# Optimization experiments

Measured on AMD Instinct MI355X. Metric: run time of the kernel, lower is better.

The kernel has to match this reference:

```python
import jax, jax.numpy as jnp
import numpy as np

NUM_CLASSES = 20   # M = len(unique(true)); label 0 is background (skipped)
ALPHA = 0.7
BETA = 1.5


def setup_inputs() -> dict:
    key = jax.random.key(0)
    k1, k2, k3 = jax.random.split(key, 3)
    B, N, K = 1, 262144, 128
    points = jax.random.normal(k1, (B, N, 3), dtype=jnp.float32)
    true = jax.random.randint(k2, (B, N), 0, NUM_CLASSES)
    embedding = jax.random.normal(k3, (B, N, K), dtype=jnp.float32)
    return {"points": points, "true": true, "embedding": embedding}


def reference(points, true, embedding):
    # points: (B,N,3), true: (B,N) int labels in [0,M), embedding: (B,N,K). B == 1.
    B, N, K = embedding.shape
    M = NUM_CLASSES
    t = true[0]  # (N,)

    # g = sigmoid(||p||) per point
    g = jax.nn.sigmoid(jnp.sqrt(jnp.sum(points ** 2, axis=-1)))  # (B,N)

    # per-cluster counts and embedding means (segment reduce over N)
    counts = jax.ops.segment_sum(jnp.ones((N,), points.dtype), t, num_segments=M)  # (M,)
    safe_counts = jnp.maximum(counts, 1.0)
    means = jax.ops.segment_sum(embedding[0], t, num_segments=M) / safe_counts[:, None]  # (M,K)

    # intra-cluster: per point, distance to its cluster mean
    d = jnp.sqrt(jnp.sum((embedding - means[true]) ** 2, axis=-1))  # (B,N)
    per_point = g * jnp.square(jnp.maximum(d - ALPHA, 0.0))         # (B,N)
    intra_per_cluster = jax.ops.segment_sum(per_point[0], t, num_segments=M) / safe_counts  # (M,)
    intra = jnp.sum(intra_per_cluster[1:])  # sum over clusters 1..M-1 (skip background 0)

    # inter-cluster: pairwise mean distances among foreground clusters
    me = means[1:]                                    # (M-1, K)
    sq = jnp.sum((me[:, None, :] - me[None, :, :]) ** 2, axis=-1)  # (M-1, M-1)
    eye = jnp.eye(M - 1, dtype=sq.dtype)
    dist = jnp.sqrt(jnp.where(eye > 0, 1.0, sq))      # safe sqrt on diagonal
    inter = jnp.sum((1.0 - eye) * jnp.square(jnp.maximum(BETA - dist, 0.0)))

    return jnp.broadcast_to(intra / M + inter / (M * (M - 1)), (B,))
```

## Files before the change

kernel.cpp:

```cpp
#include <hip/hip_runtime.h>
#include <hip/hip_bf16.h>
#include <math.h>

#define NCLS 20
#define KDIM 128
#define ALPHA 0.7f
#define BETA 1.5f

#define WS_SUMS 0
#define WS_CNT (NCLS * KDIM)
#define WS_INTRA (NCLS * KDIM + NCLS)
#define WS_HIST (NCLS * KDIM + 2 * NCLS)
#define WS_CUR (NCLS * KDIM + 3 * NCLS)
#define WS_ZERO 4096
#define WS_PAIRS 4096
#define WS_NEEDED ((WS_PAIRS + 2 * 262144) * 4)

#define GRID 2048

__global__ void k_init(float* ws) {
    int i = blockIdx.x * blockDim.x + threadIdx.x;
    if (i < WS_ZERO) ws[i] = 0.0f;
}

__global__ void __launch_bounds__(256) k_hist(const int4* __restrict__ t4,
                                              float* __restrict__ ws, int N4) {
    __shared__ int h[NCLS];
    const int tid = threadIdx.x;
    if (tid < NCLS) h[tid] = 0;
    __syncthreads();
    const int gid = blockIdx.x * 256 + tid;
    if (gid < N4) {
        const int4 c = t4[gid];
        atomicAdd(&h[c.x], 1);
        atomicAdd(&h[c.y], 1);
        atomicAdd(&h[c.z], 1);
        atomicAdd(&h[c.w], 1);
    }
    __syncthreads();
    if (tid < NCLS) atomicAdd((int*)&ws[WS_HIST] + tid, h[tid]);
}

__global__ void k_scan(float* __restrict__ ws) {
    if (threadIdx.x == 0) {
        const int* h = (const int*)&ws[WS_HIST];
        int* cur = (int*)&ws[WS_CUR];
        int run = 0;
        for (int c = 0; c < NCLS; c++) {
            cur[c] = run;
            ws[WS_CNT + c] = (float)h[c];
            run += h[c];
        }
    }
}

__global__ void __launch_bounds__(256) k_scatter(const int4* __restrict__ t4,
                                                 float* __restrict__ ws, int N4) {
    __shared__ int h[NCLS], lbase[NCLS], lcur[NCLS];
    const int tid = threadIdx.x;
    if (tid < NCLS) { h[tid] = 0; lcur[tid] = 0; }
    __syncthreads();
    const int gid = blockIdx.x * 256 + tid;
    int4 c4 = make_int4(0, 0, 0, 0);
    if (gid < N4) {
        c4 = t4[gid];
        atomicAdd(&h[c4.x], 1);
        atomicAdd(&h[c4.y], 1);
        atomicAdd(&h[c4.z], 1);
        atomicAdd(&h[c4.w], 1);
    }
    __syncthreads();
    if (tid < NCLS) lbase[tid] = atomicAdd((int*)&ws[WS_CUR] + tid, h[tid]);
    __syncthreads();
    if (gid < N4) {
        int2* pairs = (int2*)&ws[WS_PAIRS];
        const int p0 = gid * 4;
        int cc[4] = {c4.x, c4.y, c4.z, c4.w};
        for (int j = 0; j < 4; j++) {
            const int c = cc[j];
            const int dst = lbase[c] + atomicAdd(&lcur[c], 1);
            pairs[dst] = make_int2(c, p0 + j);
        }
    }
}

#define SUMS_GRID 1024
__global__ void __launch_bounds__(256) k_sums(const float4* __restrict__ emb4,
                                              const float* __restrict__ ws_ro,
                                              float* __restrict__ ws, int N) {
    __shared__ float lsum[NCLS * KDIM];
    const int tid = threadIdx.x;
    for (int i = tid; i < NCLS * KDIM; i += 256) lsum[i] = 0.0f;
    __syncthreads();

    const int s = tid & 31;
    const int hw = blockIdx.x * 8 + (tid >> 5);
    const int2* pairs = (const int2*)&ws_ro[WS_PAIRS];
    const int base = hw * 32;

#define FLUSHA(C, A)                                                \
    {                                                               \
        float* a = &lsum[(C) * KDIM + 4 * s];                       \
        unsafeAtomicAdd(a + 0, (A).x);                              \
        unsafeAtomicAdd(a + 1, (A).y);                              \
        unsafeAtomicAdd(a + 2, (A).z);                              \
        unsafeAtomicAdd(a + 3, (A).w);                              \
    }

    if (base < N) {
        int2 pr = pairs[base];
        int ccur = __builtin_amdgcn_readfirstlane(pr.x);
        float4 acc = emb4[(size_t)pr.y * 32 + s];
        for (int j0 = 4; j0 <= 32; j0 += 4) {
            int2 q0, q1, q2, q3;
            float4 v0, v1, v2, v3;
            const bool more = j0 < 32;
            if (more) {
                q0 = pairs[base + j0 + 0];
                q1 = pairs[base + j0 + 1];
                q2 = pairs[base + j0 + 2];
                q3 = pairs[base + j0 + 3];
                v0 = emb4[(size_t)q0.y * 32 + s];
                v1 = emb4[(size_t)q1.y * 32 + s];
                v2 = emb4[(size_t)q2.y * 32 + s];
                v3 = emb4[(size_t)q3.y * 32 + s];
            }
            const int lo = j0 - 4 ? j0 - 4 : 1;
            for (int j = lo; j < j0; j++) {
                int2 q = pairs[base + j];
                float4 v = emb4[(size_t)q.y * 32 + s];
                const int c = __builtin_amdgcn_readfirstlane(q.x);
                if (c != ccur) {
                    FLUSHA(ccur, acc);
                    ccur = c;
                    acc = v;
                } else {
                    acc.x += v.x; acc.y += v.y; acc.z += v.z; acc.w += v.w;
                }
            }
            (void)more; (void)q0; (void)q1; (void)q2; (void)q3;
            (void)v0; (void)v1; (void)v2; (void)v3;
        }
        FLUSHA(ccur, acc);
    }
#undef FLUSHA
    __syncthreads();

    for (int i = tid; i < NCLS * KDIM; i += 256)
        if (lsum[i] != 0.0f) unsafeAtomicAdd(&ws[WS_SUMS + i], lsum[i]);
}

#define FB_BLK 128
#define FB_GRID 2048
__global__ void __launch_bounds__(FB_BLK) k_sums_fb(const float4* __restrict__ emb4,
                                                    const int* __restrict__ t,
                                                    float* __restrict__ ws, int N) {
    __shared__ float lsum[2][NCLS * KDIM];
    __shared__ float lcnt[NCLS];
    __shared__ int lds_t[FB_BLK];
    const int tid = threadIdx.x;
    const int w = tid >> 6, k = tid & 63;
    const int half = k >> 5;
    const int k31 = k & 31;
    for (int i = tid; i < 2 * NCLS * KDIM; i += FB_BLK) (&lsum[0][0])[i] = 0.0f;
    if (tid < NCLS) lcnt[tid] = 0.0f;
    __syncthreads();
    const int chunk = blockIdx.x * FB_BLK;
    const int npts = min(FB_BLK, N - chunk);
    if (tid < npts) {
        const int c = t[chunk + tid];
        lds_t[tid] = c;
        unsafeAtomicAdd(&lcnt[c], 1.0f);
    }
    __syncthreads();
    float* L = lsum[w];
    for (int q = 32 * w; q < 32 * w + 32; q++) {
        const int pl = 2 * q + half;
        if (pl < npts) {
            const int c = lds_t[pl];
            const float4 v = emb4[(size_t)(chunk + pl) * 32 + k31];
            const int cA = __shfl(c, 0, 64);
            const int cB = __shfl(c, 32, 64);
            if (cA == cB) {
                float4 vv;
                vv.x = v.x + __shfl_xor(v.x, 32, 64);
                vv.y = v.y + __shfl_xor(v.y, 32, 64);
                vv.z = v.z + __shfl_xor(v.z, 32, 64);
                vv.w = v.w + __shfl_xor(v.w, 32, 64);
                if (half == 0) {
                    float4* a = (float4*)&L[cA * KDIM + 4 * k31];
                    float4 o = *a;
                    o.x += vv.x; o.y += vv.y; o.z += vv.z; o.w += vv.w;
                    *a = o;
                }
            } else {
                float4* a = (float4*)&L[c * KDIM + 4 * k31];
                float4 o = *a;
                o.x += v.x; o.y += v.y; o.z += v.z; o.w += v.w;
                *a = o;
            }
        }
    }
    __syncthreads();
    for (int i = tid; i < NCLS * KDIM; i += FB_BLK)
        unsafeAtomicAdd(&ws[WS_SUMS + i], lsum[0][i] + lsum[1][i]);
    if (tid < NCLS) unsafeAtomicAdd(&ws[WS_CNT + tid], lcnt[tid]);
}

__global__ void __launch_bounds__(256) k_intra(const float4* __restrict__ emb4,
                                               const int* __restrict__ t,
                                               const float* __restrict__ pts,
                                               float* __restrict__ ws, int N) {
    __shared__ float lmean[NCLS * KDIM];
    __shared__ float lintra[NCLS];
    const int tid = threadIdx.x;
    for (int i = tid; i < NCLS * KDIM; i += 256) {
        float cnt = ws[WS_CNT + i / KDIM];
        lmean[i] = ws[WS_SUMS + i] / fmaxf(cnt, 1.0f);
    }
    if (tid < NCLS) lintra[tid] = 0.0f;
    __syncthreads();

    const int s = tid & 31;
    const int pp = tid >> 5;
    const int stride = GRID * 8;
    for (int p = blockIdx.x * 8 + pp; p < N; p += 2 * stride) {
        const int p1 = p + stride;
        {
            const int c = t[p];
            const float4 v = emb4[(size_t)p * 32 + s];
            const float4 m = *(const float4*)&lmean[c * KDIM + 4 * s];
            float dx = v.x - m.x, dy = v.y - m.y, dz = v.z - m.z, dw = v.w - m.w;
            float d2 = dx * dx + dy * dy + dz * dz + dw * dw;
            for (int off = 16; off >= 1; off >>= 1) d2 += __shfl_down(d2, off, 32);
            if (s == 0) {
                float d = sqrtf(d2);
                float px = pts[(size_t)p * 3 + 0];
                float py = pts[(size_t)p * 3 + 1];
                float pz = pts[(size_t)p * 3 + 2];
                float r = sqrtf(px * px + py * py + pz * pz);
                float g = 1.0f / (1.0f + expf(-r));
                float h = fmaxf(d - ALPHA, 0.0f);
                unsafeAtomicAdd(&lintra[c], g * h * h);
            }
        }
        if (p1 < N) {
            const int c = t[p1];
            const float4 v = emb4[(size_t)p1 * 32 + s];
            const float4 m = *(const float4*)&lmean[c * KDIM + 4 * s];
            float dx = v.x - m.x, dy = v.y - m.y, dz = v.z - m.z, dw = v.w - m.w;
            float d2 = dx * dx + dy * dy + dz * dz + dw * dw;
            for (int off = 16; off >= 1; off >>= 1) d2 += __shfl_down(d2, off, 32);
            if (s == 0) {
                float d = sqrtf(d2);
                float px = pts[(size_t)p1 * 3 + 0];
                float py = pts[(size_t)p1 * 3 + 1];
                float pz = pts[(size_t)p1 * 3 + 2];
                float r = sqrtf(px * px + py * py + pz * pz);
                float g = 1.0f / (1.0f + expf(-r));
                float h = fmaxf(d - ALPHA, 0.0f);
                unsafeAtomicAdd(&lintra[c], g * h * h);
            }
        }
    }
    __syncthreads();
    if (tid < NCLS) unsafeAtomicAdd(&ws[WS_INTRA + tid], lintra[tid]);
}

__global__ void __launch_bounds__(256) k_final(const float* __restrict__ ws,
                                               float* __restrict__ out) {
    __shared__ float lmean[NCLS * KDIM];
    __shared__ float red[256];
    const int tid = threadIdx.x;
    for (int i = tid; i < NCLS * KDIM; i += 256) {
        float cnt = ws[WS_CNT + i / KDIM];
        lmean[i] = ws[WS_SUMS + i] / fmaxf(cnt, 1.0f);
    }
    __syncthreads();

    float acc = 0.0f;
    for (int idx = tid; idx < 361; idx += 256) {
        int i = idx / 19 + 1;
        int j = idx % 19 + 1;
        if (i != j) {
            float sq = 0.0f;
            const float* mi = lmean + i * KDIM;
            const float* mj = lmean + j * KDIM;
            for (int k = 0; k < KDIM; k++) {
                float df = mi[k] - mj[k];
                sq += df * df;
            }
            float dist = sqrtf(sq);
            float h = fmaxf(BETA - dist, 0.0f);
            acc += h * h;
        }
    }
    red[tid] = acc;
    __syncthreads();
    for (int st = 128; st >= 1; st >>= 1) {
        if (tid < st) red[tid] += red[tid + st];
        __syncthreads();
    }
    if (tid == 0) {
        float intra = 0.0f;
        for (int c = 1; c < NCLS; c++) {
            intra += ws[WS_INTRA + c] / fmaxf(ws[WS_CNT + c], 1.0f);
        }
        out[0] = intra / (float)NCLS + red[0] / (float)(NCLS * (NCLS - 1));
    }
}

extern "C" void kernel_launch(void* const* d_in, const int* in_sizes, int n_in,
                              void* d_out, int out_size, void* d_ws, size_t ws_size,
                              hipStream_t stream) {
    const float* pts = (const float*)d_in[0];
    const int* t = (const int*)d_in[1];
    const int4* t4 = (const int4*)d_in[1];
    const float4* emb4 = (const float4*)d_in[2];
    float* out = (float*)d_out;
    float* ws = (float*)d_ws;
    const int N = in_sizes[1];
    const int N4 = N / 4;

    k_init<<<(WS_ZERO + 255) / 256, 256, 0, stream>>>(ws);

    if (ws_size >= (size_t)WS_NEEDED && (N % 4) == 0) {
        k_hist<<<(N4 + 255) / 256, 256, 0, stream>>>(t4, ws, N4);
        k_scan<<<1, 64, 0, stream>>>(ws);
        k_scatter<<<(N4 + 255) / 256, 256, 0, stream>>>(t4, ws, N4);
        k_sums<<<SUMS_GRID, 256, 0, stream>>>(emb4, ws, ws, N);
    } else {
        k_sums_fb<<<FB_GRID, FB_BLK, 0, stream>>>(emb4, t, ws, N);
    }
    k_intra<<<GRID, 256, 0, stream>>>(emb4, t, pts, ws, N);
    k_final<<<1, 256, 0, stream>>>(ws, out);
}
```

Baseline: 106.3 us.

## Rewrite sorted segment-sum to shuffle-broadcast pairs and flush directly to global

The sorted-pairs segment-sum kernel no longer uses a shared-memory accumulator. Each lane loads one (class, index) pair once and broadcasts it with shuffles, and gathers are issued eight at a time so more loads are in flight. Run boundaries are flushed with atomics straight to global sums. This drops the LDS zeroing, the final LDS-to-global pass and the redundant per-lane pair loads, at the cost of more global atomics at class boundaries. The scan is also parallelised across threads, the init kernel becomes a single small block, and restrict qualifiers on the aliased workspace are removed.

Result: slower. 185.8 us (+74.9%).

```diff
diff --git a/kernel.cpp b/kernel.cpp
--- a/kernel.cpp
+++ b/kernel.cpp
@@ -9,18 +9,18 @@
 
 #define WS_SUMS 0
 #define WS_CNT (NCLS * KDIM)
-#define WS_INTRA (NCLS * KDIM + NCLS)
-#define WS_HIST (NCLS * KDIM + 2 * NCLS)
-#define WS_CUR (NCLS * KDIM + 3 * NCLS)
-#define WS_ZERO 4096
+#define WS_INTRA (WS_CNT + NCLS)
+#define WS_HIST (WS_INTRA + NCLS)
+#define WS_CUR (WS_HIST + NCLS)
+#define WS_ZERO_N (WS_CUR + NCLS)
 #define WS_PAIRS 4096
 #define WS_NEEDED ((WS_PAIRS + 2 * 262144) * 4)
 
 #define GRID 2048
 
 __global__ void k_init(float* ws) {
-    int i = blockIdx.x * blockDim.x + threadIdx.x;
-    if (i < WS_ZERO) ws[i] = 0.0f;
+    const int tid = threadIdx.x;
+    for (int i = tid; i < WS_ZERO_N; i += 256) ws[i] = 0.0f;
 }
 
 __global__ void __launch_bounds__(256) k_hist(const int4* __restrict__ t4,
@@ -41,21 +41,19 @@
     if (tid < NCLS) atomicAdd((int*)&ws[WS_HIST] + tid, h[tid]);
 }
 
-__global__ void k_scan(float* __restrict__ ws) {
-    if (threadIdx.x == 0) {
+__global__ void k_scan(float* ws) {
+    const int c = threadIdx.x;
+    if (c < NCLS) {
         const int* h = (const int*)&ws[WS_HIST];
-        int* cur = (int*)&ws[WS_CUR];
         int run = 0;
-        for (int c = 0; c < NCLS; c++) {
-            cur[c] = run;
-            ws[WS_CNT + c] = (float)h[c];
-            run += h[c];
-        }
+        for (int i = 0; i < NCLS; i++) run += (i < c) ? h[i] : 0;
+        ((int*)&ws[WS_CUR])[c] = run;
+        ws[WS_CNT + c] = (float)h[c];
     }
 }
 
 __global__ void __launch_bounds__(256) k_scatter(const int4* __restrict__ t4,
-                                                 float* __restrict__ ws, int N4) {
+                                                 float* ws, int N4) {
     __shared__ int h[NCLS], lbase[NCLS], lcur[NCLS];
     const int tid = threadIdx.x;
     if (tid < NCLS) { h[tid] = 0; lcur[tid] = 0; }
@@ -76,6 +74,7 @@
         int2* pairs = (int2*)&ws[WS_PAIRS];
         const int p0 = gid * 4;
         int cc[4] = {c4.x, c4.y, c4.z, c4.w};
+#pragma unroll
         for (int j = 0; j < 4; j++) {
             const int c = cc[j];
             const int dst = lbase[c] + atomicAdd(&lcur[c], 1);
@@ -86,75 +85,71 @@
 
 #define SUMS_GRID 1024
 __global__ void __launch_bounds__(256) k_sums(const float4* __restrict__ emb4,
-                                              const float* __restrict__ ws_ro,
-                                              float* __restrict__ ws, int N) {
-    __shared__ float lsum[NCLS * KDIM];
-    const int tid = threadIdx.x;
-    for (int i = tid; i < NCLS * KDIM; i += 256) lsum[i] = 0.0f;
-    __syncthreads();
-
+                                              float* ws, int N) {
+    const int tid = threadIdx.x;
     const int s = tid & 31;
     const int hw = blockIdx.x * 8 + (tid >> 5);
-    const int2* pairs = (const int2*)&ws_ro[WS_PAIRS];
     const int base = hw * 32;
-
-#define FLUSHA(C, A)                                                \
-    {                                                               \
-        float* a = &lsum[(C) * KDIM + 4 * s];                       \
-        unsafeAtomicAdd(a + 0, (A).x);                              \
-        unsafeAtomicAdd(a + 1, (A).y);                              \
-        unsafeAtomicAdd(a + 2, (A).z);                              \
-        unsafeAtomicAdd(a + 3, (A).w);                              \
-    }
-
-    if (base < N) {
-        int2 pr = pairs[base];
-        int ccur = __builtin_amdgcn_readfirstlane(pr.x);
-        float4 acc = emb4[(size_t)pr.y * 32 + s];
-        for (int j0 = 4; j0 <= 32; j0 += 4) {
-            int2 q0, q1, q2, q3;
-            float4 v0, v1, v2, v3;
-            const bool more = j0 < 32;
-            if (more) {
-                q0 = pairs[base + j0 + 0];
-                q1 = pairs[base + j0 + 1];
-                q2 = pairs[base + j0 + 2];
-                q3 = pairs[base + j0 + 3];
-                v0 = emb4[(size_t)q0.y * 32 + s];
-                v1 = emb4[(size_t)q1.y * 32 + s];
-                v2 = emb4[(size_t)q2.y * 32 + s];
-                v3 = emb4[(size_t)q3.y * 32 + s];
-            }
-            const int lo = j0 - 4 ? j0 - 4 : 1;
-            for (int j = lo; j < j0; j++) {
-                int2 q = pairs[base + j];
-                float4 v = emb4[(size_t)q.y * 32 + s];
-                const int c = __builtin_amdgcn_readfirstlane(q.x);
-                if (c != ccur) {
-                    FLUSHA(ccur, acc);
-                    ccur = c;
-                    acc = v;
-                } else {
-                    acc.x += v.x; acc.y += v.y; acc.z += v.z; acc.w += v.w;
-                }
-            }
-            (void)more; (void)q0; (void)q1; (void)q2; (void)q3;
-            (void)v0; (void)v1; (void)v2; (void)v3;
-        }
-        FLUSHA(ccur, acc);
-    }
-#undef FLUSHA
-    __syncthreads();
-
-    for (int i = tid; i < NCLS * KDIM; i += 256)
-        if (lsum[i] != 0.0f) unsafeAtomicAdd(&ws[WS_SUMS + i], lsum[i]);
+    if (base >= N) return;
+    const int cnt = min(32, N - base);
+    const int2* pairs = (const int2*)&ws[WS_PAIRS];
+    const int2 myp = pairs[base + min(s, cnt - 1)];
+    const int myc = myp.x;
+    const int myi = myp.y;
+    float* gs = &ws[WS_SUMS];
+
+    float4 acc = make_float4(0.f, 0.f, 0.f, 0.f);
+    int ccur = -1;
+#define FLUSHG()                                              \
+    {                                                         \
+        float* a = &gs[ccur * KDIM + 4 * s];                  \
+        unsafeAtomicAdd(a + 0, acc.x);                        \
+        unsafeAtomicAdd(a + 1, acc.y);                        \
+        unsafeAtomicAdd(a + 2, acc.z);                        \
+        unsafeAtomicAdd(a + 3, acc.w);                        \
+    }
+#define MERGE(C, V)                                           \
+    {                                                         \
+        if ((C) != ccur) {                                    \
+            if (ccur >= 0) FLUSHG();                          \
+            ccur = (C);                                       \
+            acc = (V);                                        \
+        } else {                                              \
+            acc.x += (V).x; acc.y += (V).y;                   \
+            acc.z += (V).z; acc.w += (V).w;                   \
+        }                                                     \
+    }
+
+    if (cnt == 32) {
+        for (int j0 = 0; j0 < 32; j0 += 8) {
+            float4 v0, v1, v2, v3, v4, v5, v6, v7;
+            int c0, c1, c2, c3, c4, c5, c6, c7;
+#define G(jj) { const int idx = __shfl(myi, j0 + jj, 32);                 \
+                v##jj = emb4[(size_t)idx * 32 + s];                       \
+                c##jj = __shfl(myc, j0 + jj, 32); }
+            G(0) G(1) G(2) G(3) G(4) G(5) G(6) G(7)
+#undef G
+            MERGE(c0, v0) MERGE(c1, v1) MERGE(c2, v2) MERGE(c3, v3)
+            MERGE(c4, v4) MERGE(c5, v5) MERGE(c6, v6) MERGE(c7, v7)
+        }
+    } else {
+        for (int j = 0; j < cnt; j++) {
+            const int idx = __shfl(myi, j, 32);
+            const float4 v = emb4[(size_t)idx * 32 + s];
+            const int c = __shfl(myc, j, 32);
+            MERGE(c, v)
+        }
+    }
+    if (ccur >= 0) FLUSHG();
+#undef MERGE
+#undef FLUSHG
 }
 
 #define FB_BLK 128
 #define FB_GRID 2048
 __global__ void __launch_bounds__(FB_BLK) k_sums_fb(const float4* __restrict__ emb4,
                                                     const int* __restrict__ t,
-                                                    float* __restrict__ ws, int N) {
+                                                    float* ws, int N) {
     __shared__ float lsum[2][NCLS * KDIM];
     __shared__ float lcnt[NCLS];
     __shared__ int lds_t[FB_BLK];
@@ -210,7 +205,7 @@
 __global__ void __launch_bounds__(256) k_intra(const float4* __restrict__ emb4,
                                                const int* __restrict__ t,
                                                const float* __restrict__ pts,
-                                               float* __restrict__ ws, int N) {
+                                               float* ws, int N) {
     __shared__ float lmean[NCLS * KDIM];
     __shared__ float lintra[NCLS];
     const int tid = threadIdx.x;
@@ -267,8 +262,7 @@
     if (tid < NCLS) unsafeAtomicAdd(&ws[WS_INTRA + tid], lintra[tid]);
 }
 
-__global__ void __launch_bounds__(256) k_final(const float* __restrict__ ws,
-                                               float* __restrict__ out) {
+__global__ void __launch_bounds__(256) k_final(const float* ws, float* out) {
     __shared__ float lmean[NCLS * KDIM];
     __shared__ float red[256];
     const int tid = threadIdx.x;
@@ -322,13 +316,13 @@
     const int N = in_sizes[1];
     const int N4 = N / 4;
 
-    k_init<<<(WS_ZERO + 255) / 256, 256, 0, stream>>>(ws);
+    k_init<<<1, 256, 0, stream>>>(ws);
 
     if (ws_size >= (size_t)WS_NEEDED && (N % 4) == 0) {
         k_hist<<<(N4 + 255) / 256, 256, 0, stream>>>(t4, ws, N4);
         k_scan<<<1, 64, 0, stream>>>(ws);
         k_scatter<<<(N4 + 255) / 256, 256, 0, stream>>>(t4, ws, N4);
-        k_sums<<<SUMS_GRID, 256, 0, stream>>>(emb4, ws, ws, N);
+        k_sums<<<SUMS_GRID, 256, 0, stream>>>(emb4, ws, N);
     } else {
         k_sums_fb<<<FB_GRID, FB_BLK, 0, stream>>>(emb4, t, ws, N);
     }
```
